# Optimization experiments

Measured on AMD Instinct MI355X. Metric: run time of the kernel, lower is better.

## Reference

```python
import jax, jax.numpy as jnp
import numpy as np

EPS = 1e-5
HEADS, DIM_HEAD = 8, 64


def rmsnorm(x, g):
    # einn.Norm('b... [d]', mean=False, bias=False): rms-normalize last dim, learned scale
    return x * jax.lax.rsqrt(jnp.mean(jnp.square(x), axis=-1, keepdims=True) + EPS) * g


def setup_inputs() -> dict:
    key = jax.random.key(0)
    ks = jax.random.split(key, 10)
    B, N, D, DE, H, DH = 1, 1024, 512, 64, HEADS, DIM_HEAD
    s = 0.02
    return {
        'x': jax.random.normal(ks[0], (B, N, D), jnp.float32),
        'mask': jnp.ones((B, N), dtype=bool),
        'edges': jax.random.normal(ks[1], (B, N, N, DE), jnp.float32),
        'rms_g': jnp.ones((D,), jnp.float32),
        'w_qkv': jax.random.normal(ks[2], (D, 3 * H * DH), jnp.float32) * s,
        'w_gates': jax.random.normal(ks[3], (D, H), jnp.float32) * s,
        'b_gates': jnp.zeros((H,), jnp.float32),
        'edges_rms_g': jnp.ones((DE,), jnp.float32),
        'w_eb': jax.random.normal(ks[4], (DE, H), jnp.float32) * s,
        'b_eb': jnp.zeros((H,), jnp.float32),
        'w_th': jnp.eye(H, dtype=jnp.float32) + jax.random.normal(ks[5], (H, H), jnp.float32) * s,
        'w_out': jax.random.normal(ks[6], (H * DH, D), jnp.float32) * s,
        'w_eout': jax.random.normal(ks[7], (H, DE), jnp.float32) * s,
    }


def reference(x, mask, edges, rms_g, w_qkv, w_gates, b_gates, edges_rms_g, w_eb, b_eb, w_th, w_out, w_eout):
    B, N, D = x.shape
    H, DH = HEADS, DIM_HEAD
    scale = DH ** 0.5  # NOTE: source multiplies q by dim_head**0.5 (faithful)

    xn = rmsnorm(x, rms_g)
    qkv = (xn @ w_qkv).reshape(B, N, 3, H, DH)
    q = jnp.transpose(qkv[:, :, 0], (0, 2, 1, 3)) * scale  # b h n d
    k = jnp.transpose(qkv[:, :, 1], (0, 2, 1, 3))
    v = jnp.transpose(qkv[:, :, 2], (0, 2, 1, 3))

    sim = jnp.einsum('bhid,bhjd->bhij', q, k)
    # edge bias: rmsnorm -> Linear(dim_edges, heads) -> b h i j
    bias = jnp.einsum('bije,eh->bhij', rmsnorm(edges, edges_rms_g), w_eb) + b_eb[None, :, None, None]
    sim = sim + bias
    # pre talking heads: Conv2d(H, H, 1, bias=False)
    sim = jnp.einsum('bhij,gh->bgij', sim, w_th)

    mask_value = -jnp.finfo(sim.dtype).max
    sim = jnp.where(mask[:, None, None, :], sim, mask_value)

    attn = jax.nn.softmax(sim, axis=-1)
    out = jnp.einsum('bhij,bhjd->bhid', attn, v)

    gates = jax.nn.sigmoid(xn @ w_gates + b_gates)  # b n h
    out = out * jnp.transpose(gates, (0, 2, 1))[..., None]  # b h n 1

    out = jnp.transpose(out, (0, 2, 1, 3)).reshape(B, N, H * DH) @ w_out  # b n dim
    edges_out = jnp.einsum('bhij,he->bije', attn, w_eout)  # Conv2d(H, DE, 1) then b d i j -> b i j d
    return out, edges_out
```

## Files before the change

kernel.cpp:

```cpp
#include <hip/hip_runtime.h>
#include <math.h>

#define EPS 1e-5f

__global__ __launch_bounds__(256) void prep_kernel(
    const float* __restrict__ w_th, const float* __restrict__ w_eb,
    const float* __restrict__ b_eb, const float* __restrict__ erg,
    float* __restrict__ G2, float* __restrict__ b2)
{
  int t = threadIdx.x;
  for (int idx = t; idx < 512; idx += 256) {
    int g = idx >> 6, d = idx & 63;
    float s = 0.f;
#pragma unroll
    for (int h = 0; h < 8; ++h) s += w_th[g * 8 + h] * w_eb[d * 8 + h];
    G2[idx] = erg[d] * s;
  }
  if (t < 8) {
    float s = 0.f;
#pragma unroll
    for (int h = 0; h < 8; ++h) s += w_th[t * 8 + h] * b_eb[h];
    b2[t] = s;
  }
}

__global__ __launch_bounds__(256) void rms_gates_kernel(
    const float* __restrict__ x, const float* __restrict__ rms_g,
    const float* __restrict__ w_gates, const float* __restrict__ b_gates,
    float* __restrict__ xn, float* __restrict__ gates)
{
  int i = blockIdx.x, t = threadIdx.x;
  __shared__ float red[256];
  float2 v = *(const float2*)&x[i * 512 + t * 2];
  red[t] = v.x * v.x + v.y * v.y;
  __syncthreads();
  for (int s = 128; s > 0; s >>= 1) {
    if (t < s) red[t] += red[t + s];
    __syncthreads();
  }
  float ssq = red[0];
  __syncthreads();
  float inv = rsqrtf(ssq * (1.0f / 512.0f) + EPS);
  float x0 = v.x * inv * rms_g[t * 2];
  float x1 = v.y * inv * rms_g[t * 2 + 1];
  float2 o; o.x = x0; o.y = x1;
  *(float2*)&xn[i * 512 + t * 2] = o;

  float ph[8];
#pragma unroll
  for (int h = 0; h < 8; ++h)
    ph[h] = x0 * w_gates[(t * 2) * 8 + h] + x1 * w_gates[(t * 2 + 1) * 8 + h];
  for (int h = 0; h < 8; ++h) {
    red[t] = ph[h];
    __syncthreads();
    for (int s = 128; s > 0; s >>= 1) {
      if (t < s) red[t] += red[t + s];
      __syncthreads();
    }
    if (t == 0) {
      float z = red[0] + b_gates[h];
      gates[i * 8 + h] = 1.0f / (1.0f + __expf(-z));
    }
    __syncthreads();
  }
}

__global__ __launch_bounds__(256) void gemm_f32(
    const float* __restrict__ A, const float* __restrict__ B, float* __restrict__ C,
    int M, int N, int K)
{
  __shared__ float As[16][68];
  __shared__ float Bs[16][68];
  int t = threadIdx.x;
  int bn = blockIdx.x, bm = blockIdx.y;
  int row0 = bm * 64, col0 = bn * 64;
  int tm = t & 15, tn = t >> 4;
  int ar = t >> 2, ac = (t & 3) * 4;
  int br = t >> 4, bc = (t & 15) * 4;
  float acc[4][4] = {};
  for (int k0 = 0; k0 < K; k0 += 16) {
    float4 av = *(const float4*)&A[(size_t)(row0 + ar) * K + k0 + ac];
    float4 bv = *(const float4*)&B[(size_t)(k0 + br) * N + col0 + bc];
    __syncthreads();
    As[ac + 0][ar] = av.x; As[ac + 1][ar] = av.y; As[ac + 2][ar] = av.z; As[ac + 3][ar] = av.w;
    *(float4*)&Bs[br][bc] = bv;
    __syncthreads();
#pragma unroll
    for (int k = 0; k < 16; ++k) {
      float4 a = *(const float4*)&As[k][tm * 4];
      float4 b = *(const float4*)&Bs[k][tn * 4];
      acc[0][0] += a.x * b.x; acc[0][1] += a.x * b.y; acc[0][2] += a.x * b.z; acc[0][3] += a.x * b.w;
      acc[1][0] += a.y * b.x; acc[1][1] += a.y * b.y; acc[1][2] += a.y * b.z; acc[1][3] += a.y * b.w;
      acc[2][0] += a.z * b.x; acc[2][1] += a.z * b.y; acc[2][2] += a.z * b.z; acc[2][3] += a.z * b.w;
      acc[3][0] += a.w * b.x; acc[3][1] += a.w * b.y; acc[3][2] += a.w * b.z; acc[3][3] += a.w * b.w;
    }
  }
#pragma unroll
  for (int aa = 0; aa < 4; ++aa) {
    float4 o; o.x = acc[aa][0]; o.y = acc[aa][1]; o.z = acc[aa][2]; o.w = acc[aa][3];
    *(float4*)&C[(size_t)(row0 + tm * 4 + aa) * N + col0 + tn * 4] = o;
  }
}

__global__ __launch_bounds__(256) void qk_kernel(
    const float* __restrict__ qkv, float* __restrict__ sim)
{
  int jt = blockIdx.x, it = blockIdx.y, h = blockIdx.z;
  __shared__ float Qs[16][68];
  __shared__ float Ks[16][68];
  int t = threadIdx.x;
  int tm = t & 15, tn = t >> 4;
  int r = t >> 2, c4 = (t & 3) * 4;
  const float* qb = qkv + h * 64;
  const float* kb = qkv + 512 + h * 64;
  float acc[4][4] = {};
  for (int k0 = 0; k0 < 64; k0 += 16) {
    float4 qv = *(const float4*)&qb[(size_t)(it * 64 + r) * 1536 + k0 + c4];
    float4 kv = *(const float4*)&kb[(size_t)(jt * 64 + r) * 1536 + k0 + c4];
    __syncthreads();
    Qs[c4 + 0][r] = qv.x * 8.0f; Qs[c4 + 1][r] = qv.y * 8.0f; Qs[c4 + 2][r] = qv.z * 8.0f; Qs[c4 + 3][r] = qv.w * 8.0f;
    Ks[c4 + 0][r] = kv.x; Ks[c4 + 1][r] = kv.y; Ks[c4 + 2][r] = kv.z; Ks[c4 + 3][r] = kv.w;
    __syncthreads();
#pragma unroll
    for (int k = 0; k < 16; ++k) {
      float4 a = *(const float4*)&Qs[k][tm * 4];
      float4 b = *(const float4*)&Ks[k][tn * 4];
      acc[0][0] += a.x * b.x; acc[0][1] += a.x * b.y; acc[0][2] += a.x * b.z; acc[0][3] += a.x * b.w;
      acc[1][0] += a.y * b.x; acc[1][1] += a.y * b.y; acc[1][2] += a.y * b.z; acc[1][3] += a.y * b.w;
      acc[2][0] += a.z * b.x; acc[2][1] += a.z * b.y; acc[2][2] += a.z * b.z; acc[2][3] += a.z * b.w;
      acc[3][0] += a.w * b.x; acc[3][1] += a.w * b.y; acc[3][2] += a.w * b.z; acc[3][3] += a.w * b.w;
    }
  }
#pragma unroll
  for (int aa = 0; aa < 4; ++aa) {
    float4 o; o.x = acc[aa][0]; o.y = acc[aa][1]; o.z = acc[aa][2]; o.w = acc[aa][3];
    *(float4*)&sim[((size_t)h << 20) + (size_t)(it * 64 + tm * 4 + aa) * 1024 + jt * 64 + tn * 4] = o;
  }
}

__global__ __launch_bounds__(256) void attn_fused(
    float* simattn,
    const float* __restrict__ edges,
    const float* __restrict__ w_th,
    const float* __restrict__ G2,
    const float* __restrict__ b2,
    const float* __restrict__ w_eout,
    float* __restrict__ edges_out)
{
  __shared__ float lg[8 * 1024];
  int i = blockIdx.x, t = threadIdx.x;

  for (int idx = t; idx < 8192; idx += 256) {
    int h = idx >> 10, j = idx & 1023;
    lg[idx] = simattn[((size_t)h << 20) + ((size_t)i << 10) + j];
  }
  __syncthreads();

  float tmp[4][8];
#pragma unroll
  for (int c = 0; c < 4; ++c) {
    int j = t + 256 * c;
    float l[8];
#pragma unroll
    for (int h = 0; h < 8; ++h) l[h] = lg[h * 1024 + j];
#pragma unroll
    for (int g = 0; g < 8; ++g) {
      float s = 0.f;
#pragma unroll
      for (int h = 0; h < 8; ++h) s += w_th[g * 8 + h] * l[h];
      tmp[c][g] = s;
    }
  }
  __syncthreads();
#pragma unroll
  for (int c = 0; c < 4; ++c) {
    int j = t + 256 * c;
#pragma unroll
    for (int g = 0; g < 8; ++g) lg[g * 1024 + j] = tmp[c][g];
  }
  __syncthreads();

  const float* erow = edges + (size_t)i * (1024 * 64);
  for (int c = 0; c < 4; ++c) {
    int j = t + 256 * c;
    const float* ep = erow + j * 64;
    float e[64];
#pragma unroll
    for (int q4 = 0; q4 < 16; ++q4) {
      float4 v = *(const float4*)(ep + q4 * 4);
      e[q4 * 4 + 0] = v.x; e[q4 * 4 + 1] = v.y; e[q4 * 4 + 2] = v.z; e[q4 * 4 + 3] = v.w;
    }
    float ssq = 0.f;
#pragma unroll
    for (int d = 0; d < 64; ++d) ssq += e[d] * e[d];
    float r = rsqrtf(ssq * (1.0f / 64.0f) + EPS);
#pragma unroll
    for (int g = 0; g < 8; ++g) {
      float s = 0.f;
#pragma unroll
      for (int d = 0; d < 64; ++d) s += e[d] * G2[g * 64 + d];
      lg[g * 1024 + j] += s * r + b2[g];
    }
  }
  __syncthreads();

  {
    int g = t >> 5, l = t & 31;
    float mx = -1e30f;
    for (int c2 = 0; c2 < 32; ++c2) mx = fmaxf(mx, lg[g * 1024 + l + 32 * c2]);
#pragma unroll
    for (int off = 16; off >= 1; off >>= 1) mx = fmaxf(mx, __shfl_down(mx, off, 32));
    mx = __shfl(mx, 0, 32);
    float sum = 0.f;
    for (int c2 = 0; c2 < 32; ++c2) {
      int idx = g * 1024 + l + 32 * c2;
      float ev = __expf(lg[idx] - mx);
      lg[idx] = ev;
      sum += ev;
    }
#pragma unroll
    for (int off = 16; off >= 1; off >>= 1) sum += __shfl_down(sum, off, 32);
    sum = __shfl(sum, 0, 32);
    float inv = 1.0f / sum;
    for (int c2 = 0; c2 < 32; ++c2) lg[g * 1024 + l + 32 * c2] *= inv;
  }
  __syncthreads();

  for (int idx = t; idx < 8192; idx += 256) {
    int h = idx >> 10, j = idx & 1023;
    simattn[((size_t)h << 20) + ((size_t)i << 10) + j] = lg[idx];
  }
  for (int c = 0; c < 4; ++c) {
    int j = t + 256 * c;
    float a[8];
#pragma unroll
    for (int gg = 0; gg < 8; ++gg) a[gg] = lg[gg * 1024 + j];
    float* eop = edges_out + ((size_t)(i * 1024 + j)) * 64;
#pragma unroll
    for (int e4 = 0; e4 < 16; ++e4) {
      float4 acc; acc.x = 0.f; acc.y = 0.f; acc.z = 0.f; acc.w = 0.f;
#pragma unroll
      for (int gg = 0; gg < 8; ++gg) {
        float av = a[gg];
        acc.x += av * w_eout[gg * 64 + e4 * 4 + 0];
        acc.y += av * w_eout[gg * 64 + e4 * 4 + 1];
        acc.z += av * w_eout[gg * 64 + e4 * 4 + 2];
        acc.w += av * w_eout[gg * 64 + e4 * 4 + 3];
      }
      *(float4*)(eop + e4 * 4) = acc;
    }
  }
}

__global__ __launch_bounds__(256) void av_kernel(
    const float* __restrict__ attn, const float* __restrict__ qkv,
    const float* __restrict__ gates, float* __restrict__ outh)
{
  int it = blockIdx.y, g = blockIdx.z;
  __shared__ float As[16][68];
  __shared__ float Bs[16][68];
  int t = threadIdx.x;
  int tm = t & 15, tn = t >> 4;
  int ar = t >> 2, ac = (t & 3) * 4;
  int br = t >> 4, bc = (t & 15) * 4;
  const float* Ab = attn + ((size_t)g << 20) + (size_t)(it * 64) * 1024;
  const float* Bb = qkv + 1024 + g * 64;
  float acc[4][4] = {};
  for (int k0 = 0; k0 < 1024; k0 += 16) {
    float4 av = *(const float4*)&Ab[(size_t)ar * 1024 + k0 + ac];
    float4 bv = *(const float4*)&Bb[(size_t)(k0 + br) * 1536 + bc];
    __syncthreads();
    As[ac + 0][ar] = av.x; As[ac + 1][ar] = av.y; As[ac + 2][ar] = av.z; As[ac + 3][ar] = av.w;
    *(float4*)&Bs[br][bc] = bv;
    __syncthreads();
#pragma unroll
    for (int k = 0; k < 16; ++k) {
      float4 a = *(const float4*)&As[k][tm * 4];
      float4 b = *(const float4*)&Bs[k][tn * 4];
      acc[0][0] += a.x * b.x; acc[0][1] += a.x * b.y; acc[0][2] += a.x * b.z; acc[0][3] += a.x * b.w;
      acc[1][0] += a.y * b.x; acc[1][1] += a.y * b.y; acc[1][2] += a.y * b.z; acc[1][3] += a.y * b.w;
      acc[2][0] += a.z * b.x; acc[2][1] += a.z * b.y; acc[2][2] += a.z * b.z; acc[2][3] += a.z * b.w;
      acc[3][0] += a.w * b.x; acc[3][1] += a.w * b.y; acc[3][2] += a.w * b.z; acc[3][3] += a.w * b.w;
    }
  }
#pragma unroll
  for (int aa = 0; aa < 4; ++aa) {
    int irow = it * 64 + tm * 4 + aa;
    float gt = gates[irow * 8 + g];
    float4 o; o.x = acc[aa][0] * gt; o.y = acc[aa][1] * gt; o.z = acc[aa][2] * gt; o.w = acc[aa][3] * gt;
    *(float4*)&outh[(size_t)irow * 512 + g * 64 + tn * 4] = o;
  }
}

extern "C" void kernel_launch(void* const* d_in, const int* in_sizes, int n_in,
                              void* d_out, int out_size, void* d_ws, size_t ws_size,
                              hipStream_t stream) {
  const float* x       = (const float*)d_in[0];
  const float* edges   = (const float*)d_in[2];
  const float* rms_g   = (const float*)d_in[3];
  const float* w_qkv   = (const float*)d_in[4];
  const float* w_gates = (const float*)d_in[5];
  const float* b_gates = (const float*)d_in[6];
  const float* erg     = (const float*)d_in[7];
  const float* w_eb    = (const float*)d_in[8];
  const float* b_eb    = (const float*)d_in[9];
  const float* w_th    = (const float*)d_in[10];
  const float* w_out   = (const float*)d_in[11];
  const float* w_eout  = (const float*)d_in[12];

  float* out = (float*)d_out;
  float* eo  = out + 1024 * 512;

  float* ws    = (float*)d_ws;
  float* xn    = ws;
  float* gates = xn + 524288;
  float* qkv   = gates + 8192;
  float* sim   = qkv + 1572864;
  float* outh  = sim + 8388608;
  float* G2    = outh + 524288;
  float* b2    = G2 + 512;

  prep_kernel<<<1, 256, 0, stream>>>(w_th, w_eb, b_eb, erg, G2, b2);
  rms_gates_kernel<<<1024, 256, 0, stream>>>(x, rms_g, w_gates, b_gates, xn, gates);
  gemm_f32<<<dim3(1536 / 64, 1024 / 64), 256, 0, stream>>>(xn, w_qkv, qkv, 1024, 1536, 512);
  qk_kernel<<<dim3(16, 16, 8), 256, 0, stream>>>(qkv, sim);
  attn_fused<<<1024, 256, 0, stream>>>(sim, edges, w_th, G2, b2, w_eout, eo);
  av_kernel<<<dim3(1, 16, 8), 256, 0, stream>>>(sim, qkv, gates, outh);
  gemm_f32<<<dim3(512 / 64, 1024 / 64), 256, 0, stream>>>(outh, w_out, out, 1024, 512, 512);
}
```

Before: 729.0 us.

## Restructure attention kernel, shrink GEMM tiles, prefetch loads, warp-shuffle RMS reductions

The fused attention kernel now stages edges through a padded shared-memory tile so global reads are coalesced. It computes the logits in registers and runs the softmax with wave shuffles, and the edges_out writes are spread across 16 threads per row with w_eout held in registers. The GEMM and AV kernels move to 32-row tiles to double the number of blocks, and they prefetch the next k-slice into registers. The rmsnorm/gates kernel replaces its tree reductions with wave shuffles and folds the normalization scale in after the reduction. Together these target uncoalesced edge reads, low occupancy in the small-grid kernels, and barrier overhead, at the cost of more register pressure and less reuse per tile.

```diff
diff --git a/kernel.cpp b/kernel.cpp
--- a/kernel.cpp
+++ b/kernel.cpp
@@ -30,75 +30,84 @@
     float* __restrict__ xn, float* __restrict__ gates)
 {
   int i = blockIdx.x, t = threadIdx.x;
-  __shared__ float red[256];
+  __shared__ float red[4][9];
   float2 v = *(const float2*)&x[i * 512 + t * 2];
-  red[t] = v.x * v.x + v.y * v.y;
+  float g0 = rms_g[t * 2], g1 = rms_g[t * 2 + 1];
+  float a0 = v.x * g0, a1 = v.y * g1;
+  float ssq = v.x * v.x + v.y * v.y;
+  float4 wa = *(const float4*)&w_gates[t * 16 + 0];
+  float4 wb = *(const float4*)&w_gates[t * 16 + 4];
+  float4 wc = *(const float4*)&w_gates[t * 16 + 8];
+  float4 wd = *(const float4*)&w_gates[t * 16 + 12];
+  float ph[8];
+  ph[0] = a0 * wa.x + a1 * wc.x; ph[1] = a0 * wa.y + a1 * wc.y;
+  ph[2] = a0 * wa.z + a1 * wc.z; ph[3] = a0 * wa.w + a1 * wc.w;
+  ph[4] = a0 * wb.x + a1 * wd.x; ph[5] = a0 * wb.y + a1 * wd.y;
+  ph[6] = a0 * wb.z + a1 * wd.z; ph[7] = a0 * wb.w + a1 * wd.w;
+#pragma unroll
+  for (int off = 32; off >= 1; off >>= 1) {
+    ssq += __shfl_xor(ssq, off, 64);
+#pragma unroll
+    for (int h = 0; h < 8; ++h) ph[h] += __shfl_xor(ph[h], off, 64);
+  }
+  int wv = t >> 6;
+  if ((t & 63) == 0) {
+    red[wv][0] = ssq;
+#pragma unroll
+    for (int h = 0; h < 8; ++h) red[wv][1 + h] = ph[h];
+  }
   __syncthreads();
-  for (int s = 128; s > 0; s >>= 1) {
-    if (t < s) red[t] += red[t + s];
-    __syncthreads();
-  }
-  float ssq = red[0];
-  __syncthreads();
-  float inv = rsqrtf(ssq * (1.0f / 512.0f) + EPS);
-  float x0 = v.x * inv * rms_g[t * 2];
-  float x1 = v.y * inv * rms_g[t * 2 + 1];
-  float2 o; o.x = x0; o.y = x1;
+  float ssqT = red[0][0] + red[1][0] + red[2][0] + red[3][0];
+  float inv = rsqrtf(ssqT * (1.0f / 512.0f) + EPS);
+  float2 o; o.x = v.x * inv * g0; o.y = v.y * inv * g1;
   *(float2*)&xn[i * 512 + t * 2] = o;
-
-  float ph[8];
-#pragma unroll
-  for (int h = 0; h < 8; ++h)
-    ph[h] = x0 * w_gates[(t * 2) * 8 + h] + x1 * w_gates[(t * 2 + 1) * 8 + h];
-  for (int h = 0; h < 8; ++h) {
-    red[t] = ph[h];
-    __syncthreads();
-    for (int s = 128; s > 0; s >>= 1) {
-      if (t < s) red[t] += red[t + s];
-      __syncthreads();
-    }
-    if (t == 0) {
-      float z = red[0] + b_gates[h];
-      gates[i * 8 + h] = 1.0f / (1.0f + __expf(-z));
-    }
-    __syncthreads();
-  }
-}
-
-__global__ __launch_bounds__(256) void gemm_f32(
+  if (t < 8) {
+    float p = red[0][1 + t] + red[1][1 + t] + red[2][1 + t] + red[3][1 + t];
+    float z = p * inv + b_gates[t];
+    gates[i * 8 + t] = 1.0f / (1.0f + __expf(-z));
+  }
+}
+
+__global__ __launch_bounds__(256) void gemm32_f32(
     const float* __restrict__ A, const float* __restrict__ B, float* __restrict__ C,
     int M, int N, int K)
 {
-  __shared__ float As[16][68];
+  __shared__ float As[16][40];
   __shared__ float Bs[16][68];
   int t = threadIdx.x;
-  int bn = blockIdx.x, bm = blockIdx.y;
-  int row0 = bm * 64, col0 = bn * 64;
-  int tm = t & 15, tn = t >> 4;
+  int row0 = blockIdx.y * 32, col0 = blockIdx.x * 64;
+  int tm = t & 7, tn = t >> 3;
   int ar = t >> 2, ac = (t & 3) * 4;
   int br = t >> 4, bc = (t & 15) * 4;
-  float acc[4][4] = {};
+  float4 av, bv;
+  if (t < 128) av = *(const float4*)&A[(size_t)(row0 + ar) * K + ac];
+  bv = *(const float4*)&B[(size_t)br * N + col0 + bc];
+  float acc[4][2] = {};
   for (int k0 = 0; k0 < K; k0 += 16) {
-    float4 av = *(const float4*)&A[(size_t)(row0 + ar) * K + k0 + ac];
-    float4 bv = *(const float4*)&B[(size_t)(k0 + br) * N + col0 + bc];
-    __syncthreads();
-    As[ac + 0][ar] = av.x; As[ac + 1][ar] = av.y; As[ac + 2][ar] = av.z; As[ac + 3][ar] = av.w;
+    __syncthreads();
+    if (t < 128) {
+      As[ac + 0][ar] = av.x; As[ac + 1][ar] = av.y; As[ac + 2][ar] = av.z; As[ac + 3][ar] = av.w;
+    }
     *(float4*)&Bs[br][bc] = bv;
     __syncthreads();
+    if (k0 + 16 < K) {
+      if (t < 128) av = *(const float4*)&A[(size_t)(row0 + ar) * K + k0 + 16 + ac];
+      bv = *(const float4*)&B[(size_t)(k0 + 16 + br) * N + col0 + bc];
+    }
 #pragma unroll
     for (int k = 0; k < 16; ++k) {
       float4 a = *(const float4*)&As[k][tm * 4];
-      float4 b = *(const float4*)&Bs[k][tn * 4];
-      acc[0][0] += a.x * b.x; acc[0][1] += a.x * b.y; acc[0][2] += a.x * b.z; acc[0][3] += a.x * b.w;
-      acc[1][0] += a.y * b.x; acc[1][1] += a.y * b.y; acc[1][2] += a.y * b.z; acc[1][3] += a.y * b.w;
-      acc[2][0] += a.z * b.x; acc[2][1] += a.z * b.y; acc[2][2] += a.z * b.z; acc[2][3] += a.z * b.w;
-      acc[3][0] += a.w * b.x; acc[3][1] += a.w * b.y; acc[3][2] += a.w * b.z; acc[3][3] += a.w * b.w;
+      float2 b = *(const float2*)&Bs[k][tn * 2];
+      acc[0][0] += a.x * b.x; acc[0][1] += a.x * b.y;
+      acc[1][0] += a.y * b.x; acc[1][1] += a.y * b.y;
+      acc[2][0] += a.z * b.x; acc[2][1] += a.z * b.y;
+      acc[3][0] += a.w * b.x; acc[3][1] += a.w * b.y;
     }
   }
 #pragma unroll
   for (int aa = 0; aa < 4; ++aa) {
-    float4 o; o.x = acc[aa][0]; o.y = acc[aa][1]; o.z = acc[aa][2]; o.w = acc[aa][3];
-    *(float4*)&C[(size_t)(row0 + tm * 4 + aa) * N + col0 + tn * 4] = o;
+    float2 o; o.x = acc[aa][0]; o.y = acc[aa][1];
+    *(float2*)&C[(size_t)(row0 + tm * 4 + aa) * N + col0 + tn * 2] = o;
   }
 }
 
@@ -113,14 +122,18 @@
   int r = t >> 2, c4 = (t & 3) * 4;
   const float* qb = qkv + h * 64;
   const float* kb = qkv + 512 + h * 64;
+  float4 qv = *(const float4*)&qb[(size_t)(it * 64 + r) * 1536 + c4];
+  float4 kv = *(const float4*)&kb[(size_t)(jt * 64 + r) * 1536 + c4];
   float acc[4][4] = {};
   for (int k0 = 0; k0 < 64; k0 += 16) {
-    float4 qv = *(const float4*)&qb[(size_t)(it * 64 + r) * 1536 + k0 + c4];
-    float4 kv = *(const float4*)&kb[(size_t)(jt * 64 + r) * 1536 + k0 + c4];
     __syncthreads();
     Qs[c4 + 0][r] = qv.x * 8.0f; Qs[c4 + 1][r] = qv.y * 8.0f; Qs[c4 + 2][r] = qv.z * 8.0f; Qs[c4 + 3][r] = qv.w * 8.0f;
     Ks[c4 + 0][r] = kv.x; Ks[c4 + 1][r] = kv.y; Ks[c4 + 2][r] = kv.z; Ks[c4 + 3][r] = kv.w;
     __syncthreads();
+    if (k0 + 16 < 64) {
+      qv = *(const float4*)&qb[(size_t)(it * 64 + r) * 1536 + k0 + 16 + c4];
+      kv = *(const float4*)&kb[(size_t)(jt * 64 + r) * 1536 + k0 + 16 + c4];
+    }
 #pragma unroll
     for (int k = 0; k < 16; ++k) {
       float4 a = *(const float4*)&Qs[k][tm * 4];
@@ -138,8 +151,8 @@
   }
 }
 
-__global__ __launch_bounds__(256) void attn_fused(
-    float* simattn,
+__global__ __launch_bounds__(256) void attn_fused2(
+    float* __restrict__ simattn,
     const float* __restrict__ edges,
     const float* __restrict__ w_th,
     const float* __restrict__ G2,
@@ -147,108 +160,130 @@
     const float* __restrict__ w_eout,
     float* __restrict__ edges_out)
 {
-  __shared__ float lg[8 * 1024];
+  __shared__ float lg[8192];
+  __shared__ float tile[256 * 17];
+  __shared__ float red[4][8];
   int i = blockIdx.x, t = threadIdx.x;
-
-  for (int idx = t; idx < 8192; idx += 256) {
-    int h = idx >> 10, j = idx & 1023;
-    lg[idx] = simattn[((size_t)h << 20) + ((size_t)i << 10) + j];
-  }
-  __syncthreads();
-
-  float tmp[4][8];
-#pragma unroll
-  for (int c = 0; c < 4; ++c) {
-    int j = t + 256 * c;
+  int wv = t >> 6;
+  int sub = t & 15, grp = t >> 4;
+
+  float weo[8][4];
+#pragma unroll
+  for (int g = 0; g < 8; ++g) {
+    float4 v = *(const float4*)&w_eout[g * 64 + sub * 4];
+    weo[g][0] = v.x; weo[g][1] = v.y; weo[g][2] = v.z; weo[g][3] = v.w;
+  }
+  float b2r[8];
+#pragma unroll
+  for (int g = 0; g < 8; ++g) b2r[g] = b2[g];
+
+  const float* erow = edges + (size_t)i * 65536;
+  float lgv[4][8];
+  float vmax[8];
+#pragma unroll
+  for (int g = 0; g < 8; ++g) vmax[g] = -1e30f;
+
+  for (int jg = 0; jg < 4; ++jg) {
+    float ssq = 0.f;
+    float dot[8] = {0.f, 0.f, 0.f, 0.f, 0.f, 0.f, 0.f, 0.f};
+    for (int dc = 0; dc < 4; ++dc) {
+      __syncthreads();
+#pragma unroll
+      for (int it = 0; it < 4; ++it) {
+        int lin = t + 256 * it;
+        int jr = lin >> 2, c = lin & 3;
+        float4 v = *(const float4*)&erow[(size_t)(jg * 256 + jr) * 64 + dc * 16 + c * 4];
+        tile[jr * 17 + c * 4 + 0] = v.x;
+        tile[jr * 17 + c * 4 + 1] = v.y;
+        tile[jr * 17 + c * 4 + 2] = v.z;
+        tile[jr * 17 + c * 4 + 3] = v.w;
+      }
+      __syncthreads();
+#pragma unroll
+      for (int d = 0; d < 16; ++d) {
+        float e = tile[t * 17 + d];
+        ssq += e * e;
+        int dd = dc * 16 + d;
+#pragma unroll
+        for (int g = 0; g < 8; ++g) dot[g] += e * G2[g * 64 + dd];
+      }
+    }
+    int j = jg * 256 + t;
     float l[8];
 #pragma unroll
-    for (int h = 0; h < 8; ++h) l[h] = lg[h * 1024 + j];
+    for (int h = 0; h < 8; ++h) l[h] = simattn[((size_t)h << 20) + ((size_t)i << 10) + j];
+    float r = rsqrtf(ssq * (1.0f / 64.0f) + EPS);
 #pragma unroll
     for (int g = 0; g < 8; ++g) {
       float s = 0.f;
 #pragma unroll
       for (int h = 0; h < 8; ++h) s += w_th[g * 8 + h] * l[h];
-      tmp[c][g] = s;
-    }
+      s += dot[g] * r + b2r[g];
+      lgv[jg][g] = s;
+      vmax[g] = fmaxf(vmax[g], s);
+    }
+  }
+#pragma unroll
+  for (int g = 0; g < 8; ++g) {
+#pragma unroll
+    for (int off = 32; off >= 1; off >>= 1) vmax[g] = fmaxf(vmax[g], __shfl_xor(vmax[g], off, 64));
+  }
+  if ((t & 63) == 0) {
+#pragma unroll
+    for (int g = 0; g < 8; ++g) red[wv][g] = vmax[g];
   }
   __syncthreads();
-#pragma unroll
-  for (int c = 0; c < 4; ++c) {
-    int j = t + 256 * c;
-#pragma unroll
-    for (int g = 0; g < 8; ++g) lg[g * 1024 + j] = tmp[c][g];
-  }
+  float mx[8];
+#pragma unroll
+  for (int g = 0; g < 8; ++g)
+    mx[g] = fmaxf(fmaxf(red[0][g], red[1][g]), fmaxf(red[2][g], red[3][g]));
   __syncthreads();
-
-  const float* erow = edges + (size_t)i * (1024 * 64);
-  for (int c = 0; c < 4; ++c) {
-    int j = t + 256 * c;
-    const float* ep = erow + j * 64;
-    float e[64];
-#pragma unroll
-    for (int q4 = 0; q4 < 16; ++q4) {
-      float4 v = *(const float4*)(ep + q4 * 4);
-      e[q4 * 4 + 0] = v.x; e[q4 * 4 + 1] = v.y; e[q4 * 4 + 2] = v.z; e[q4 * 4 + 3] = v.w;
-    }
-    float ssq = 0.f;
-#pragma unroll
-    for (int d = 0; d < 64; ++d) ssq += e[d] * e[d];
-    float r = rsqrtf(ssq * (1.0f / 64.0f) + EPS);
+  float vsum[8] = {0.f, 0.f, 0.f, 0.f, 0.f, 0.f, 0.f, 0.f};
+#pragma unroll
+  for (int jg = 0; jg < 4; ++jg) {
+    int j = jg * 256 + t;
 #pragma unroll
     for (int g = 0; g < 8; ++g) {
-      float s = 0.f;
-#pragma unroll
-      for (int d = 0; d < 64; ++d) s += e[d] * G2[g * 64 + d];
-      lg[g * 1024 + j] += s * r + b2[g];
-    }
+      float ev = __expf(lgv[jg][g] - mx[g]);
+      lgv[jg][g] = ev;
+      lg[g * 1024 + j] = ev;
+      vsum[g] += ev;
+    }
+  }
+#pragma unroll
+  for (int g = 0; g < 8; ++g) {
+#pragma unroll
+    for (int off = 32; off >= 1; off >>= 1) vsum[g] += __shfl_xor(vsum[g], off, 64);
+  }
+  if ((t & 63) == 0) {
+#pragma unroll
+    for (int g = 0; g < 8; ++g) red[wv][g] = vsum[g];
   }
   __syncthreads();
-
-  {
-    int g = t >> 5, l = t & 31;
-    float mx = -1e30f;
-    for (int c2 = 0; c2 < 32; ++c2) mx = fmaxf(mx, lg[g * 1024 + l + 32 * c2]);
-#pragma unroll
-    for (int off = 16; off >= 1; off >>= 1) mx = fmaxf(mx, __shfl_down(mx, off, 32));
-    mx = __shfl(mx, 0, 32);
-    float sum = 0.f;
-    for (int c2 = 0; c2 < 32; ++c2) {
-      int idx = g * 1024 + l + 32 * c2;
-      float ev = __expf(lg[idx] - mx);
-      lg[idx] = ev;
-      sum += ev;
-    }
-#pragma unroll
-    for (int off = 16; off >= 1; off >>= 1) sum += __shfl_down(sum, off, 32);
-    sum = __shfl(sum, 0, 32);
-    float inv = 1.0f / sum;
-    for (int c2 = 0; c2 < 32; ++c2) lg[g * 1024 + l + 32 * c2] *= inv;
-  }
-  __syncthreads();
-
-  for (int idx = t; idx < 8192; idx += 256) {
-    int h = idx >> 10, j = idx & 1023;
-    simattn[((size_t)h << 20) + ((size_t)i << 10) + j] = lg[idx];
-  }
-  for (int c = 0; c < 4; ++c) {
-    int j = t + 256 * c;
+  float inv[8];
+#pragma unroll
+  for (int g = 0; g < 8; ++g)
+    inv[g] = 1.0f / (red[0][g] + red[1][g] + red[2][g] + red[3][g]);
+#pragma unroll
+  for (int jg = 0; jg < 4; ++jg) {
+    int j = jg * 256 + t;
+#pragma unroll
+    for (int g = 0; g < 8; ++g)
+      simattn[((size_t)g << 20) + ((size_t)i << 10) + j] = lgv[jg][g] * inv[g];
+  }
+  for (int pass = 0; pass < 64; ++pass) {
+    int j = pass * 16 + grp;
     float a[8];
 #pragma unroll
-    for (int gg = 0; gg < 8; ++gg) a[gg] = lg[gg * 1024 + j];
-    float* eop = edges_out + ((size_t)(i * 1024 + j)) * 64;
-#pragma unroll
-    for (int e4 = 0; e4 < 16; ++e4) {
-      float4 acc; acc.x = 0.f; acc.y = 0.f; acc.z = 0.f; acc.w = 0.f;
-#pragma unroll
-      for (int gg = 0; gg < 8; ++gg) {
-        float av = a[gg];
-        acc.x += av * w_eout[gg * 64 + e4 * 4 + 0];
-        acc.y += av * w_eout[gg * 64 + e4 * 4 + 1];
-        acc.z += av * w_eout[gg * 64 + e4 * 4 + 2];
-        acc.w += av * w_eout[gg * 64 + e4 * 4 + 3];
-      }
-      *(float4*)(eop + e4 * 4) = acc;
-    }
+    for (int g = 0; g < 8; ++g) a[g] = lg[g * 1024 + j] * inv[g];
+    float4 o;
+    o.x = a[0] * weo[0][0]; o.y = a[0] * weo[0][1]; o.z = a[0] * weo[0][2]; o.w = a[0] * weo[0][3];
+#pragma unroll
+    for (int g = 1; g < 8; ++g) {
+      o.x += a[g] * weo[g][0]; o.y += a[g] * weo[g][1];
+      o.z += a[g] * weo[g][2]; o.w += a[g] * weo[g][3];
+    }
+    *(float4*)&edges_out[((size_t)(i * 1024 + j)) * 64 + sub * 4] = o;
   }
 }
 
@@ -257,38 +292,45 @@
     const float* __restrict__ gates, float* __restrict__ outh)
 {
   int it = blockIdx.y, g = blockIdx.z;
-  __shared__ float As[16][68];
+  __shared__ float As[16][40];
   __shared__ float Bs[16][68];
   int t = threadIdx.x;
-  int tm = t & 15, tn = t >> 4;
+  int tm = t & 7, tn = t >> 3;
   int ar = t >> 2, ac = (t & 3) * 4;
   int br = t >> 4, bc = (t & 15) * 4;
-  const float* Ab = attn + ((size_t)g << 20) + (size_t)(it * 64) * 1024;
+  const float* Ab = attn + ((size_t)g << 20) + (size_t)(it * 32) * 1024;
   const float* Bb = qkv + 1024 + g * 64;
-  float acc[4][4] = {};
+  float4 av, bv;
+  if (t < 128) av = *(const float4*)&Ab[(size_t)ar * 1024 + ac];
+  bv = *(const float4*)&Bb[(size_t)br * 1536 + bc];
+  float acc[4][2] = {};
   for (int k0 = 0; k0 < 1024; k0 += 16) {
-    float4 av = *(const float4*)&Ab[(size_t)ar * 1024 + k0 + ac];
-    float4 bv = *(const float4*)&Bb[(size_t)(k0 + br) * 1536 + bc];
-    __syncthreads();
-    As[ac + 0][ar] = av.x; As[ac + 1][ar] = av.y; As[ac + 2][ar] = av.z; As[ac + 3][ar] = av.w;
+    __syncthreads();
+    if (t < 128) {
+      As[ac + 0][ar] = av.x; As[ac + 1][ar] = av.y; As[ac + 2][ar] = av.z; As[ac + 3][ar] = av.w;
+    }
     *(float4*)&Bs[br][bc] = bv;
     __syncthreads();
+    if (k0 + 16 < 1024) {
+      if (t < 128) av = *(const float4*)&Ab[(size_t)ar * 1024 + k0 + 16 + ac];
+      bv = *(const float4*)&Bb[(size_t)(k0 + 16 + br) * 1536 + bc];
+    }
 #pragma unroll
     for (int k = 0; k < 16; ++k) {
       float4 a = *(const float4*)&As[k][tm * 4];
-      float4 b = *(const float4*)&Bs[k][tn * 4];
-      acc[0][0] += a.x * b.x; acc[0][1] += a.x * b.y; acc[0][2] += a.x * b.z; acc[0][3] += a.x * b.w;
-      acc[1][0] += a.y * b.x; acc[1][1] += a.y * b.y; acc[1][2] += a.y * b.z; acc[1][3] += a.y * b.w;
-      acc[2][0] += a.z * b.x; acc[2][1] += a.z * b.y; acc[2][2] += a.z * b.z; acc[2][3] += a.z * b.w;
-      acc[3][0] += a.w * b.x; acc[3][1] += a.w * b.y; acc[3][2] += a.w * b.z; acc[3][3] += a.w * b.w;
+      float2 b = *(const float2*)&Bs[k][tn * 2];
+      acc[0][0] += a.x * b.x; acc[0][1] += a.x * b.y;
+      acc[1][0] += a.y * b.x; acc[1][1] += a.y * b.y;
+      acc[2][0] += a.z * b.x; acc[2][1] += a.z * b.y;
+      acc[3][0] += a.w * b.x; acc[3][1] += a.w * b.y;
     }
   }
 #pragma unroll
   for (int aa = 0; aa < 4; ++aa) {
-    int irow = it * 64 + tm * 4 + aa;
+    int irow = it * 32 + tm * 4 + aa;
     float gt = gates[irow * 8 + g];
-    float4 o; o.x = acc[aa][0] * gt; o.y = acc[aa][1] * gt; o.z = acc[aa][2] * gt; o.w = acc[aa][3] * gt;
-    *(float4*)&outh[(size_t)irow * 512 + g * 64 + tn * 4] = o;
+    float2 o; o.x = acc[aa][0] * gt; o.y = acc[aa][1] * gt;
+    *(float2*)&outh[(size_t)irow * 512 + g * 64 + tn * 2] = o;
   }
 }
 
@@ -322,9 +364,9 @@
 
   prep_kernel<<<1, 256, 0, stream>>>(w_th, w_eb, b_eb, erg, G2, b2);
   rms_gates_kernel<<<1024, 256, 0, stream>>>(x, rms_g, w_gates, b_gates, xn, gates);
-  gemm_f32<<<dim3(1536 / 64, 1024 / 64), 256, 0, stream>>>(xn, w_qkv, qkv, 1024, 1536, 512);
+  gemm32_f32<<<dim3(1536 / 64, 1024 / 32), 256, 0, stream>>>(xn, w_qkv, qkv, 1024, 1536, 512);
   qk_kernel<<<dim3(16, 16, 8), 256, 0, stream>>>(qkv, sim);
-  attn_fused<<<1024, 256, 0, stream>>>(sim, edges, w_th, G2, b2, w_eout, eo);
-  av_kernel<<<dim3(1, 16, 8), 256, 0, stream>>>(sim, qkv, gates, outh);
-  gemm_f32<<<dim3(512 / 64, 1024 / 64), 256, 0, stream>>>(outh, w_out, out, 1024, 512, 512);
-}
+  attn_fused2<<<1024, 256, 0, stream>>>(sim, edges, w_th, G2, b2, w_eout, eo);
+  av_kernel<<<dim3(1, 32, 8), 256, 0, stream>>>(sim, qkv, gates, outh);
+  gemm32_f32<<<dim3(512 / 64, 1024 / 32), 256, 0, stream>>>(outh, w_out, out, 1024, 512, 512);
+}
```

Result: faster. 679.9 us (-6.7%).
